# Performance work log

Measured on AMD Instinct MI355X. Metric: run time of the kernel, lower is better.

Reference implementation:

```python
import jax, jax.numpy as jnp
import numpy as np

B, N, E = 16384, 25, 64
IN_DIM, HID, OUT = 3, 128, 128


def setup_inputs() -> dict:
    key = jax.random.key(0)
    ks = jax.random.split(key, 7)
    x = jax.random.normal(ks[0], (B, N, IN_DIM), dtype=jnp.float32)
    edge_index = jax.random.randint(ks[1], (2, E), 0, N, dtype=jnp.int64)
    # SAGEConv params: lin_l (aggregated neighbors) and lin_r (root), shared bias on lin_l
    W1_l = jax.random.normal(ks[2], (IN_DIM, HID), dtype=jnp.float32) / np.sqrt(IN_DIM)
    W1_r = jax.random.normal(ks[3], (IN_DIM, HID), dtype=jnp.float32) / np.sqrt(IN_DIM)
    b1 = jnp.zeros((HID,), dtype=jnp.float32)
    W2_l = jax.random.normal(ks[4], (HID, OUT), dtype=jnp.float32) / np.sqrt(HID)
    W2_r = jax.random.normal(ks[5], (HID, OUT), dtype=jnp.float32) / np.sqrt(HID)
    b2 = jnp.zeros((OUT,), dtype=jnp.float32)
    return {"x": x, "edge_index": edge_index, "W1_l": W1_l, "W1_r": W1_r,
            "b1": b1, "W2_l": W2_l, "W2_r": W2_r, "b2": b2}


def _sage_conv(h, src, dst, deg_inv, Wl, Wr, b):
    # h: [B, N, F]; gather sources, scatter-mean into destinations (axis 1)
    msgs = h[:, src, :]                                        # [B, E, F]
    agg = jnp.zeros_like(h).at[:, dst, :].add(msgs) * deg_inv  # [B, N, F] mean over in-edges
    return agg @ Wl + h @ Wr + b


def reference(x, edge_index, W1_l, W1_r, b1, W2_l, W2_r, b2):
    src, dst = edge_index[0], edge_index[1]
    n = x.shape[1]
    counts = jnp.zeros((n,), dtype=x.dtype).at[dst].add(1.0)
    deg_inv = (1.0 / jnp.maximum(counts, 1.0))[None, :, None]  # [1, N, 1]
    h = jax.nn.relu(_sage_conv(x, src, dst, deg_inv, W1_l, W1_r, b1))
    h = _sage_conv(h, src, dst, deg_inv, W2_l, W2_r, b2)
    return h.mean(axis=1)  # [B, OUT] mean pool over nodes
```

## Files before the change

kernel.cpp:

```cpp
#include <hip/hip_runtime.h>
#include <hip/hip_bf16.h>

#define NNODE 25
#define HID   128
#define GB    16
#define BLOCK 256
#define KTOT  256
#define SPAD  264
#define XTW   40

#define WS_WT   0
#define WS_MTB  65536
#define WS_CVEC 67584
#define WS_W1B  67712

typedef __attribute__((ext_vector_type(8))) short short8;
typedef __attribute__((ext_vector_type(4))) float f32x4;
typedef __attribute__((ext_vector_type(2))) float f32x2;

__device__ inline unsigned short f2bf(float f) {
  __hip_bfloat16 h = __float2bfloat16(f);
  unsigned short u; __builtin_memcpy(&u, &h, 2); return u;
}

#define XB(n, g) (((n)*GB + ((g) ^ ((n) & 15))) * 8)

__global__ __launch_bounds__(256) void prep(
    const float* __restrict__ W2l, const float* __restrict__ W2r,
    const float* __restrict__ W1l, const float* __restrict__ W1r,
    const int*   __restrict__ ei,  unsigned char* __restrict__ ws)
{
  const int blk = blockIdx.x, tid = threadIdx.x;
  if (blk < 128) {
    unsigned short* Wt = (unsigned short*)(ws + WS_WT);
    int i = blk*256 + tid;
    int o = i >> 8, k = i & 255;
    float v = (k < HID) ? W2l[k*HID + o] : W2r[(k-HID)*HID + o] * (1.f/NNODE);
    Wt[o*KTOT + k] = f2bf(v);
    return;
  }
  __shared__ float Mm[NNODE*NNODE];
  __shared__ float cnt[NNODE];
  for (int i = tid; i < NNODE*NNODE; i += 256) Mm[i] = 0.f;
  if (tid < NNODE) cnt[tid] = 0.f;
  __syncthreads();
  if (tid < 64) {
    int s = ei[tid], d = ei[64 + tid];
    atomicAdd(&Mm[d*NNODE + s], 1.f);
    atomicAdd(&cnt[d], 1.f);
  }
  __syncthreads();
  for (int i = tid; i < NNODE*NNODE; i += 256) {
    int n = i / NNODE;
    Mm[i] *= 1.f / fmaxf(cnt[n], 1.f);
  }
  __syncthreads();
  unsigned short* Mtb = (unsigned short*)(ws + WS_MTB);
  for (int i = tid; i < 1024; i += 256) {
    int n = i >> 5, m = i & 31;
    float v = (n < NNODE && m < NNODE) ? Mm[n*NNODE + m] : 0.f;
    Mtb[i] = f2bf(v);
  }
  if (tid < 32) {
    float a = 0.f;
    if (tid < NNODE)
      for (int n = 0; n < NNODE; ++n) a += Mm[n*NNODE + tid];
    ((float*)(ws + WS_CVEC))[tid] = a * (1.f/NNODE);
  }
  unsigned short* W1b = (unsigned short*)(ws + WS_W1B);
  for (int i = tid; i < 1024; i += 256) {
    int c = i >> 3, j = i & 7;
    float v = (j < 3) ? W1l[j*HID + c] : (j < 6) ? W1r[(j-3)*HID + c] : 0.f;
    W1b[i] = f2bf(v);
  }
}

__global__ __launch_bounds__(BLOCK, 5) void gnn_fused(
    const float* __restrict__ x,
    const float* __restrict__ b1,
    const float* __restrict__ b2,
    const unsigned char* __restrict__ ws,
    float* __restrict__ out)
{
  __shared__ __align__(16) unsigned short Mtb[32][32];
  __shared__ float cvecs[32];
  __shared__ __align__(16) unsigned short Xtb[3][GB][XTW];
  __shared__ __align__(16) unsigned short Xbf[NNODE*GB*8];
  __shared__ __align__(16) unsigned short Sbf[GB][SPAD];

  const int tid  = threadIdx.x;
  const int b0   = blockIdx.x * GB;
  const int wave = tid >> 6;
  const int lane = tid & 63;
  const int r    = lane & 15;
  const int kg   = lane >> 4;
  const f32x4 zz = {0.f, 0.f, 0.f, 0.f};

  f32x4 xv[2];
  int   i4v[2];
  #pragma unroll
  for (int t = 0; t < 2; ++t) {
    int i4 = tid + t*BLOCK;
    i4v[t] = i4;
    if (i4 < GB*75/4) xv[t] = ((const f32x4*)(x + (size_t)b0*75))[i4];
  }
  for (int i = tid; i < 512; i += BLOCK)
    ((unsigned int*)Mtb)[i] = ((const unsigned int*)(ws + WS_MTB))[i];
  if (tid < 32) cvecs[tid] = ((const float*)(ws + WS_CVEC))[tid];
  for (int i = tid; i < 3*GB*7; i += BLOCK) {
    int d = i / (GB*7), rm = i % (GB*7);
    Xtb[d][rm/7][25 + rm%7] = 0;
  }
  for (int p = tid; p < NNODE*GB; p += BLOCK)
    *(unsigned int*)&Xbf[XB(p >> 4, p & 15) + 6] = 0u;
  #pragma unroll
  for (int t = 0; t < 2; ++t) {
    if (i4v[t] < GB*75/4) {
      #pragma unroll
      for (int j = 0; j < 4; ++j) {
        int e = i4v[t]*4 + j;
        int g = e / 75, rm = e - g*75;
        int n = rm / 3, d = rm - n*3;
        unsigned short bv = f2bf(xv[t][j]);
        Xtb[d][g][n] = bv;
        Xbf[XB(n, g) + 3 + d] = bv;
      }
    }
  }
  __syncthreads();

  if (wave < 3) {
    const int d = wave;
    short8 mb0 = *(const short8*)&Mtb[r][kg*8];
    short8 mb1 = *(const short8*)&Mtb[16 + r][kg*8];
    short8 af  = *(const short8*)&Xtb[d][r][kg*8];
    f32x4 g0 = __builtin_amdgcn_mfma_f32_16x16x32_bf16(af, mb0, zz, 0, 0, 0);
    f32x4 g1 = __builtin_amdgcn_mfma_f32_16x16x32_bf16(af, mb1, zz, 0, 0, 0);
    #pragma unroll
    for (int q = 0; q < 4; ++q) {
      int g = kg*4 + q;
      Xbf[XB(r, g) + d] = f2bf(g0[q]);
      if (r < 9) Xbf[XB(16 + r, g) + d] = f2bf(g1[q]);
    }
  }
  __syncthreads();

  {
    const int c0 = wave * 32;
    const int cA = c0 + r, cB = c0 + 16 + r;
    const unsigned short* W1b = (const unsigned short*)(ws + WS_W1B);
    const short8 w1A = *(const short8*)&W1b[cA * 8];
    const short8 w1B = *(const short8*)&W1b[cB * 8];
    const short8 z8  = {0,0,0,0,0,0,0,0};
    const short8 bA0 = (kg == 0) ? w1A : z8;
    const short8 bA1 = (kg == 1) ? w1A : z8;
    const short8 bB0 = (kg == 0) ? w1B : z8;
    const short8 bB1 = (kg == 1) ? w1B : z8;
    const float biasA = b1[cA], biasB = b1[cB];
    const f32x4 cbA = {biasA, biasA, biasA, biasA};
    const f32x4 cbB = {biasB, biasB, biasB, biasB};
    f32x2 s1[4] = {}, s2[4] = {};
    for (int ng = 0; ng < 12; ++ng) {
      short8 a = *(const short8*)&Xbf[XB(2*ng + (kg & 1), r)];
      f32x4 h0e = __builtin_amdgcn_mfma_f32_16x16x32_bf16(a, bA0, cbA, 0, 0, 0);
      f32x4 h1e = __builtin_amdgcn_mfma_f32_16x16x32_bf16(a, bB0, cbB, 0, 0, 0);
      f32x4 h0o = __builtin_amdgcn_mfma_f32_16x16x32_bf16(a, bA1, cbA, 0, 0, 0);
      f32x4 h1o = __builtin_amdgcn_mfma_f32_16x16x32_bf16(a, bB1, cbB, 0, 0, 0);
      const float cv0 = cvecs[2*ng], cv1 = cvecs[2*ng + 1];
      const f32x2 cvv0 = {cv0, cv0}, cvv1 = {cv1, cv1};
      #pragma unroll
      for (int q = 0; q < 4; ++q) {
        f32x2 ve; ve.x = fmaxf(h0e[q], 0.f); ve.y = fmaxf(h1e[q], 0.f);
        f32x2 vo; vo.x = fmaxf(h0o[q], 0.f); vo.y = fmaxf(h1o[q], 0.f);
        s1[q] += cvv0 * ve; s2[q] += ve;
        s1[q] += cvv1 * vo; s2[q] += vo;
      }
    }
    {
      short8 a = *(const short8*)&Xbf[XB(24, r)];
      f32x4 h0 = __builtin_amdgcn_mfma_f32_16x16x32_bf16(a, bA0, cbA, 0, 0, 0);
      f32x4 h1 = __builtin_amdgcn_mfma_f32_16x16x32_bf16(a, bB0, cbB, 0, 0, 0);
      const float cv = cvecs[24];
      const f32x2 cvv = {cv, cv};
      #pragma unroll
      for (int q = 0; q < 4; ++q) {
        f32x2 v; v.x = fmaxf(h0[q], 0.f); v.y = fmaxf(h1[q], 0.f);
        s1[q] += cvv * v;
        s2[q] += v;
      }
    }
    #pragma unroll
    for (int q = 0; q < 4; ++q) {
      int g = kg*4 + q;
      Sbf[g][cA]       = f2bf(s1[q].x);
      Sbf[g][cB]       = f2bf(s1[q].y);
      Sbf[g][HID + cA] = f2bf(s2[q].x);
      Sbf[g][HID + cB] = f2bf(s2[q].y);
    }
  }
  __syncthreads();

  {
    const int n0 = wave * 32;
    const unsigned short* Wt = (const unsigned short*)(ws + WS_WT);
    const unsigned short* WtA = Wt + (size_t)(n0 + r)      * KTOT;
    const unsigned short* WtB = Wt + (size_t)(n0 + 16 + r) * KTOT;
    f32x4 acc0 = zz, acc1 = zz;
    #pragma unroll 4
    for (int kt = 0; kt < 8; ++kt) {
      const int kb = kt*32 + kg*8;
      short8 a  = *(const short8*)&Sbf[r][kb];
      short8 bA = *(const short8*)&WtA[kb];
      short8 bB = *(const short8*)&WtB[kb];
      acc0 = __builtin_amdgcn_mfma_f32_16x16x32_bf16(a, bA, acc0, 0, 0, 0);
      acc1 = __builtin_amdgcn_mfma_f32_16x16x32_bf16(a, bB, acc1, 0, 0, 0);
    }
    const int colA = n0 + r, colB = n0 + 16 + r;
    const float bA2 = b2[colA], bB2 = b2[colB];
    #pragma unroll
    for (int q = 0; q < 4; ++q) {
      const int row = kg*4 + q;
      out[(size_t)(b0+row)*HID + colA] = acc0[q] + bA2;
      out[(size_t)(b0+row)*HID + colB] = acc1[q] + bB2;
    }
  }
}

extern "C" void kernel_launch(void* const* d_in, const int* in_sizes, int n_in,
                              void* d_out, int out_size, void* d_ws, size_t ws_size,
                              hipStream_t stream) {
  (void)n_in; (void)out_size; (void)ws_size;
  const float* x   = (const float*)d_in[0];
  const int*   ei  = (const int*)  d_in[1];
  const float* W1l = (const float*)d_in[2];
  const float* W1r = (const float*)d_in[3];
  const float* b1  = (const float*)d_in[4];
  const float* W2l = (const float*)d_in[5];
  const float* W2r = (const float*)d_in[6];
  const float* b2  = (const float*)d_in[7];
  float* out = (float*)d_out;
  unsigned char* ws = (unsigned char*)d_ws;

  const int B = in_sizes[0] / (NNODE*3);
  prep<<<dim3(129), dim3(256), 0, stream>>>(W2l, W2r, W1l, W1r, ei, ws);
  gnn_fused<<<dim3(B / GB), dim3(BLOCK), 0, stream>>>(x, b1, b2, ws, out);
}
```

Before: 23.79 us.

## Fuse prep into main kernel with global flag handshake for W2 transpose

Drops the separate prep kernel. Each block now rebuilds the adjacency mean matrix, cvec and W1 bf16 tile in shared memory, and the first 128 blocks also write the transposed bf16 W2 to the workspace. Those blocks then bump a global counter, and every block spins on that counter before the second GEMM. This removes one kernel launch and the inter-kernel gap, in exchange for redundant per-block setup work and a memset launch. It also risks deadlock if the first 128 blocks are not resident alongside the waiting blocks, though with the low block IDs scheduled first that is likely fine.

```diff
diff --git a/kernel.cpp b/kernel.cpp
--- a/kernel.cpp
+++ b/kernel.cpp
@@ -10,9 +10,7 @@
 #define XTW   40
 
 #define WS_WT   0
-#define WS_MTB  65536
-#define WS_CVEC 67584
-#define WS_W1B  67712
+#define WS_FLAG 65536
 
 typedef __attribute__((ext_vector_type(8))) short short8;
 typedef __attribute__((ext_vector_type(4))) float f32x4;
@@ -25,65 +23,23 @@
 
 #define XB(n, g) (((n)*GB + ((g) ^ ((n) & 15))) * 8)
 
-__global__ __launch_bounds__(256) void prep(
-    const float* __restrict__ W2l, const float* __restrict__ W2r,
-    const float* __restrict__ W1l, const float* __restrict__ W1r,
-    const int*   __restrict__ ei,  unsigned char* __restrict__ ws)
+__global__ __launch_bounds__(BLOCK, 5) void gnn_all(
+    const float* __restrict__ x,
+    const int*   __restrict__ ei,
+    const float* __restrict__ W1l,
+    const float* __restrict__ W1r,
+    const float* __restrict__ b1,
+    const float* __restrict__ W2l,
+    const float* __restrict__ W2r,
+    const float* __restrict__ b2,
+    unsigned char* ws,
+    float* __restrict__ out)
 {
-  const int blk = blockIdx.x, tid = threadIdx.x;
-  if (blk < 128) {
-    unsigned short* Wt = (unsigned short*)(ws + WS_WT);
-    int i = blk*256 + tid;
-    int o = i >> 8, k = i & 255;
-    float v = (k < HID) ? W2l[k*HID + o] : W2r[(k-HID)*HID + o] * (1.f/NNODE);
-    Wt[o*KTOT + k] = f2bf(v);
-    return;
-  }
   __shared__ float Mm[NNODE*NNODE];
   __shared__ float cnt[NNODE];
-  for (int i = tid; i < NNODE*NNODE; i += 256) Mm[i] = 0.f;
-  if (tid < NNODE) cnt[tid] = 0.f;
-  __syncthreads();
-  if (tid < 64) {
-    int s = ei[tid], d = ei[64 + tid];
-    atomicAdd(&Mm[d*NNODE + s], 1.f);
-    atomicAdd(&cnt[d], 1.f);
-  }
-  __syncthreads();
-  for (int i = tid; i < NNODE*NNODE; i += 256) {
-    int n = i / NNODE;
-    Mm[i] *= 1.f / fmaxf(cnt[n], 1.f);
-  }
-  __syncthreads();
-  unsigned short* Mtb = (unsigned short*)(ws + WS_MTB);
-  for (int i = tid; i < 1024; i += 256) {
-    int n = i >> 5, m = i & 31;
-    float v = (n < NNODE && m < NNODE) ? Mm[n*NNODE + m] : 0.f;
-    Mtb[i] = f2bf(v);
-  }
-  if (tid < 32) {
-    float a = 0.f;
-    if (tid < NNODE)
-      for (int n = 0; n < NNODE; ++n) a += Mm[n*NNODE + tid];
-    ((float*)(ws + WS_CVEC))[tid] = a * (1.f/NNODE);
-  }
-  unsigned short* W1b = (unsigned short*)(ws + WS_W1B);
-  for (int i = tid; i < 1024; i += 256) {
-    int c = i >> 3, j = i & 7;
-    float v = (j < 3) ? W1l[j*HID + c] : (j < 6) ? W1r[(j-3)*HID + c] : 0.f;
-    W1b[i] = f2bf(v);
-  }
-}
-
-__global__ __launch_bounds__(BLOCK, 5) void gnn_fused(
-    const float* __restrict__ x,
-    const float* __restrict__ b1,
-    const float* __restrict__ b2,
-    const unsigned char* __restrict__ ws,
-    float* __restrict__ out)
-{
+  __shared__ float cvecs[NNODE];
   __shared__ __align__(16) unsigned short Mtb[32][32];
-  __shared__ float cvecs[32];
+  __shared__ __align__(16) unsigned short W1bs[HID*8];
   __shared__ __align__(16) unsigned short Xtb[3][GB][XTW];
   __shared__ __align__(16) unsigned short Xbf[NNODE*GB*8];
   __shared__ __align__(16) unsigned short Sbf[GB][SPAD];
@@ -96,6 +52,16 @@
   const int kg   = lane >> 4;
   const f32x4 zz = {0.f, 0.f, 0.f, 0.f};
 
+  if (blockIdx.x < 128) {
+    int i = blockIdx.x*256 + tid;
+    int o = i >> 8, k = i & 255;
+    float v = (k < HID) ? W2l[k*HID + o] : W2r[(k-HID)*HID + o] * (1.f/NNODE);
+    ((unsigned short*)(ws + WS_WT))[o*KTOT + k] = f2bf(v);
+    __threadfence();
+    __syncthreads();
+    if (tid == 0) atomicAdd((unsigned int*)(ws + WS_FLAG), 1u);
+  }
+
   f32x4 xv[2];
   int   i4v[2];
   #pragma unroll
@@ -104,15 +70,28 @@
     i4v[t] = i4;
     if (i4 < GB*75/4) xv[t] = ((const f32x4*)(x + (size_t)b0*75))[i4];
   }
-  for (int i = tid; i < 512; i += BLOCK)
-    ((unsigned int*)Mtb)[i] = ((const unsigned int*)(ws + WS_MTB))[i];
-  if (tid < 32) cvecs[tid] = ((const float*)(ws + WS_CVEC))[tid];
+  for (int i = tid; i < NNODE*NNODE; i += BLOCK) Mm[i] = 0.f;
+  if (tid < NNODE) cnt[tid] = 0.f;
   for (int i = tid; i < 3*GB*7; i += BLOCK) {
     int d = i / (GB*7), rm = i % (GB*7);
     Xtb[d][rm/7][25 + rm%7] = 0;
   }
   for (int p = tid; p < NNODE*GB; p += BLOCK)
     *(unsigned int*)&Xbf[XB(p >> 4, p & 15) + 6] = 0u;
+  __syncthreads();
+
+  if (tid < 64) {
+    int s = ei[tid], d = ei[64 + tid];
+    atomicAdd(&Mm[d*NNODE + s], 1.f);
+    atomicAdd(&cnt[d], 1.f);
+  }
+  if (tid >= 64 && tid < 192) {
+    int c = tid - 64;
+    unsigned short* p = &W1bs[c*8];
+    p[0] = f2bf(W1l[c]);       p[1] = f2bf(W1l[HID+c]);  p[2] = f2bf(W1l[2*HID+c]);
+    p[3] = f2bf(W1r[c]);       p[4] = f2bf(W1r[HID+c]);  p[5] = f2bf(W1r[2*HID+c]);
+    p[6] = 0;                  p[7] = 0;
+  }
   #pragma unroll
   for (int t = 0; t < 2; ++t) {
     if (i4v[t] < GB*75/4) {
@@ -129,6 +108,17 @@
   }
   __syncthreads();
 
+  for (int i = tid; i < 1024; i += BLOCK) {
+    int n = i >> 5, m = i & 31;
+    float v = 0.f;
+    if (n < NNODE && m < NNODE) {
+      v = Mm[n*NNODE + m] / fmaxf(cnt[n], 1.f);
+      Mm[n*NNODE + m] = v;
+    }
+    ((unsigned short*)Mtb)[i] = f2bf(v);
+  }
+  __syncthreads();
+
   if (wave < 3) {
     const int d = wave;
     short8 mb0 = *(const short8*)&Mtb[r][kg*8];
@@ -142,15 +132,19 @@
       Xbf[XB(r, g) + d] = f2bf(g0[q]);
       if (r < 9) Xbf[XB(16 + r, g) + d] = f2bf(g1[q]);
     }
+  } else if (wave == 3 && lane < NNODE) {
+    float a = 0.f;
+    #pragma unroll 5
+    for (int n = 0; n < NNODE; ++n) a += Mm[n*NNODE + lane];
+    cvecs[lane] = a * (1.f/NNODE);
   }
   __syncthreads();
 
   {
     const int c0 = wave * 32;
     const int cA = c0 + r, cB = c0 + 16 + r;
-    const unsigned short* W1b = (const unsigned short*)(ws + WS_W1B);
-    const short8 w1A = *(const short8*)&W1b[cA * 8];
-    const short8 w1B = *(const short8*)&W1b[cB * 8];
+    const short8 w1A = *(const short8*)&W1bs[cA * 8];
+    const short8 w1B = *(const short8*)&W1bs[cB * 8];
     const short8 z8  = {0,0,0,0,0,0,0,0};
     const short8 bA0 = (kg == 0) ? w1A : z8;
     const short8 bA1 = (kg == 1) ? w1A : z8;
@@ -198,6 +192,12 @@
       Sbf[g][HID + cB] = f2bf(s2[q].y);
     }
   }
+
+  if (tid == 0) {
+    const unsigned int* flag = (const unsigned int*)(ws + WS_FLAG);
+    while (__hip_atomic_load(flag, __ATOMIC_ACQUIRE, __HIP_MEMORY_SCOPE_AGENT) < 128u)
+      __builtin_amdgcn_s_sleep(2);
+  }
   __syncthreads();
 
   {
@@ -242,6 +242,7 @@
   unsigned char* ws = (unsigned char*)d_ws;
 
   const int B = in_sizes[0] / (NNODE*3);
-  prep<<<dim3(129), dim3(256), 0, stream>>>(W2l, W2r, W1l, W1r, ei, ws);
-  gnn_fused<<<dim3(B / GB), dim3(BLOCK), 0, stream>>>(x, b1, b2, ws, out);
+  hipMemsetAsync(ws + WS_FLAG, 0, 4, stream);
+  gnn_all<<<dim3(B / GB), dim3(BLOCK), 0, stream>>>(
+      x, ei, W1l, W1r, b1, W2l, W2r, b2, ws, out);
 }
```

Result: slower. 55.11 us (+131.6%).
